# Kernel tuning notes

Measured on AMD Instinct MI355X. Metric: run time of the kernel, lower is better.

## Reference

```python
import jax, jax.numpy as jnp
import numpy as np

S, B, D = 128, 512, 512  # S == max_length


def setup_inputs() -> dict:
    key = jax.random.key(0)
    k1, k2 = jax.random.split(key)
    x = jax.random.normal(k1, (S, B, D), dtype=jnp.float32)
    src_mask = jax.random.bernoulli(k2, 0.2, (B, S))
    return {"x": x, "src_mask": src_mask}


def reference(x, src_mask):
    # x: (S, B, D); src_mask: (B, S) bool, True = pad.
    S_ = x.shape[0]
    xb = jnp.transpose(x, (1, 0, 2))                    # (B, S, D)
    valid = (~src_mask).astype(x.dtype)                 # (B, S)
    xm = xb * valid[:, :, None]                         # zero out padded tokens
    g = jnp.arange(S_ - 1)
    s = jnp.arange(S_)
    # left fragment g keeps positions s <= g; right keeps s > g
    keep_left = (s[None, :] <= g[:, None]).astype(x.dtype)   # (G, S)
    keep_right = jnp.asarray(1.0, x.dtype) - keep_left        # (G, S)
    left = jnp.einsum('gs,bsd->bgd', keep_left, xm)     # (B, G, D)
    right = jnp.einsum('gs,bsd->bgd', keep_right, xm)   # (B, G, D)
    return jnp.concatenate([left, right], axis=2)       # (B, G, 2D)
```

## Files before the change

kernel.cpp:

```cpp
#include <hip/hip_runtime.h>

#define SS 128
#define BB 512
#define DD 512
#define GG 127

__global__ __launch_bounds__(256) void frag_prefix_kernel(
    const float* __restrict__ x, const int* __restrict__ mask,
    float* __restrict__ out) {
  const int b = blockIdx.x >> 1;
  const int d = ((blockIdx.x & 1) << 8) + threadIdx.x;

  __shared__ float valid[SS];
  if (threadIdx.x < SS) {
    valid[threadIdx.x] = mask[b * SS + threadIdx.x] ? 0.0f : 1.0f;
  }
  __syncthreads();

  const float* xp = x + (size_t)b * DD + d;
  float v[SS];
#pragma unroll
  for (int s = 0; s < SS; ++s) {
    v[s] = xp[(size_t)s * (BB * DD)] * valid[s];
  }

  float total = 0.0f;
#pragma unroll
  for (int s = 0; s < SS; ++s) total += v[s];

  float* outp = out + (size_t)b * (GG * 2 * DD) + d;
  float run = 0.0f;
#pragma unroll
  for (int g = 0; g < GG; ++g) {
    run += v[g];
    outp[(size_t)g * (2 * DD)] = run;
    outp[(size_t)g * (2 * DD) + DD] = total - run;
  }
}

extern "C" void kernel_launch(void* const* d_in, const int* in_sizes, int n_in,
                              void* d_out, int out_size, void* d_ws, size_t ws_size,
                              hipStream_t stream) {
  const float* x = (const float*)d_in[0];
  const int* mask = (const int*)d_in[1];
  float* out = (float*)d_out;
  frag_prefix_kernel<<<dim3(BB * 2), dim3(256), 0, stream>>>(x, mask, out);
}
```

Before: 362.4 us.

## Split sequence scan across chunks with shared-memory partial sums and float4 I/O

Result: no change. 359.0 us (-0.9%).

```diff
diff --git a/kernel.cpp b/kernel.cpp
--- a/kernel.cpp
+++ b/kernel.cpp
@@ -4,37 +4,67 @@
 #define BB 512
 #define DD 512
 #define GG 127
+#define CS 16
+#define NC 8
 
-__global__ __launch_bounds__(256) void frag_prefix_kernel(
+__global__ __launch_bounds__(512) void frag_prefix_kernel(
     const float* __restrict__ x, const int* __restrict__ mask,
     float* __restrict__ out) {
+  const int tid = threadIdx.x;
   const int b = blockIdx.x >> 1;
-  const int d = ((blockIdx.x & 1) << 8) + threadIdx.x;
+  const int dblk = (blockIdx.x & 1) << 8;
+  const int col = tid & 63;
+  const int j = tid >> 6;
 
   __shared__ float valid[SS];
-  if (threadIdx.x < SS) {
-    valid[threadIdx.x] = mask[b * SS + threadIdx.x] ? 0.0f : 1.0f;
-  }
+  __shared__ float4 part[NC][64];
+
+  if (tid < SS) valid[tid] = mask[b * SS + tid] ? 0.0f : 1.0f;
   __syncthreads();
 
-  const float* xp = x + (size_t)b * DD + d;
-  float v[SS];
+  const size_t sstride = (size_t)BB * DD / 4;
+  const float4* xq = (const float4*)x +
+                     (size_t)(j * CS) * sstride +
+                     ((size_t)b * DD + dblk) / 4 + col;
+
+  float4 v[CS];
 #pragma unroll
-  for (int s = 0; s < SS; ++s) {
-    v[s] = xp[(size_t)s * (BB * DD)] * valid[s];
+  for (int i = 0; i < CS; ++i) {
+    float4 t = xq[(size_t)i * sstride];
+    float m = valid[j * CS + i];
+    v[i].x = t.x * m; v[i].y = t.y * m; v[i].z = t.z * m; v[i].w = t.w * m;
   }
 
-  float total = 0.0f;
+  float4 psum = v[0];
 #pragma unroll
-  for (int s = 0; s < SS; ++s) total += v[s];
+  for (int i = 1; i < CS; ++i) {
+    psum.x += v[i].x; psum.y += v[i].y; psum.z += v[i].z; psum.w += v[i].w;
+  }
+  part[j][col] = psum;
+  __syncthreads();
 
-  float* outp = out + (size_t)b * (GG * 2 * DD) + d;
-  float run = 0.0f;
+  float4 offset = make_float4(0.f, 0.f, 0.f, 0.f);
+  float4 total = make_float4(0.f, 0.f, 0.f, 0.f);
 #pragma unroll
-  for (int g = 0; g < GG; ++g) {
-    run += v[g];
-    outp[(size_t)g * (2 * DD)] = run;
-    outp[(size_t)g * (2 * DD) + DD] = total - run;
+  for (int jj = 0; jj < NC; ++jj) {
+    float4 p = part[jj][col];
+    total.x += p.x; total.y += p.y; total.z += p.z; total.w += p.w;
+    if (jj < j) { offset.x += p.x; offset.y += p.y; offset.z += p.z; offset.w += p.w; }
+  }
+
+  float4* op = (float4*)out + ((size_t)b * GG * 2 * DD + dblk) / 4 + col;
+  float4 run = offset;
+#pragma unroll
+  for (int i = 0; i < CS; ++i) {
+    run.x += v[i].x; run.y += v[i].y; run.z += v[i].z; run.w += v[i].w;
+    const int g = j * CS + i;
+    if (g < GG) {
+      op[(size_t)g * (2 * DD / 4)] = run;
+      float4 r;
+      r.x = total.x - run.x; r.y = total.y - run.y;
+      r.z = total.z - run.z; r.w = total.w - run.w;
+      op[(size_t)g * (2 * DD / 4) + DD / 4] = r;
+    }
   }
 }
 
@@ -44,5 +74,5 @@
   const float* x = (const float*)d_in[0];
   const int* mask = (const int*)d_in[1];
   float* out = (float*)d_out;
-  frag_prefix_kernel<<<dim3(BB * 2), dim3(256), 0, stream>>>(x, mask, out);
+  frag_prefix_kernel<<<dim3(BB * 2), dim3(512), 0, stream>>>(x, mask, out);
 }
```
